# Optimization experiments

Hardware: AMD Instinct MI355X
Metric: run time of the kernel (lower is better)

Reference implementation:

```python
import jax, jax.numpy as jnp
import numpy as np

N_USERS = 100_000
N_ITEMS = 100_000
D = 64            # args.in_size == args.out_size (GraphConv has weight=None)
N_INTENTS = 128   # hardcoded in DCCF
HID = 128         # SemanticAttention hidden_size
N_UI_EDGES = 1_000_000
N_MP_EDGES = 500_000
N_MP = 2          # metapaths per node type
B = 4096
N_LAYERS = 2      # hardcoded in DCCF


def setup_inputs() -> dict:
    key = jax.random.key(0)
    ks = jax.random.split(key, 20)
    s = 0.1
    inp = {}
    inp['user_feat'] = jax.random.normal(ks[0], (N_USERS, D), jnp.float32) * s
    inp['item_feat'] = jax.random.normal(ks[1], (N_ITEMS, D), jnp.float32) * s
    inp['user_intent'] = jax.random.normal(ks[2], (D, N_INTENTS), jnp.float32) * s
    inp['item_intent'] = jax.random.normal(ks[3], (D, N_INTENTS), jnp.float32) * s
    inp['sa_u_W1'] = jax.random.normal(ks[4], (D, HID), jnp.float32) * s
    inp['sa_u_b1'] = jnp.zeros((HID,), jnp.float32)
    inp['sa_u_w2'] = jax.random.normal(ks[5], (HID,), jnp.float32) * s
    inp['sa_i_W1'] = jax.random.normal(ks[6], (D, HID), jnp.float32) * s
    inp['sa_i_b1'] = jnp.zeros((HID,), jnp.float32)
    inp['sa_i_w2'] = jax.random.normal(ks[7], (HID,), jnp.float32) * s
    inp['ui_src'] = jax.random.randint(ks[8], (N_UI_EDGES,), 0, N_USERS)
    inp['ui_dst'] = jax.random.randint(ks[9], (N_UI_EDGES,), 0, N_ITEMS)
    inp['mp_user'] = jax.random.randint(ks[10], (N_MP, 2, N_MP_EDGES), 0, N_USERS)
    inp['mp_item'] = jax.random.randint(ks[11], (N_MP, 2, N_MP_EDGES), 0, N_ITEMS)
    # indices drawn WITHOUT replacement so torch.unique(index) in ssl_loss is a no-op
    inp['user_idx'] = jax.random.choice(ks[12], N_USERS, (B,), replace=False)
    inp['item_idx'] = jax.random.choice(ks[13], N_ITEMS, (B,), replace=False)
    inp['neg_item_idx'] = jax.random.randint(ks[14], (B,), 0, N_ITEMS)
    return inp


def _forward(user_feat, item_feat, user_intent, item_intent,
             sa_u_W1, sa_u_b1, sa_u_w2, sa_i_W1, sa_i_b1, sa_i_w2,
             ui_src, ui_dst, mp_user, mp_item, user_idx, item_idx, neg_item_idx):
    n_nodes = N_USERS + N_ITEMS
    # symmetric bipartite adjacency in COO (tmp_adj + tmp_adj.T)
    rows = jnp.concatenate([ui_src, ui_dst + N_USERS])
    cols = jnp.concatenate([ui_dst + N_USERS, ui_src])
    deg = jnp.maximum(jax.ops.segment_sum(jnp.ones_like(rows, jnp.float32), rows,
                                          num_segments=n_nodes), 1.0)
    dinv = jax.lax.rsqrt(deg)
    gv = dinv[rows] * dinv[cols]  # G = D^{-1/2} A D^{-1/2}

    def spmm(x):  # gather-scale-scatter, the torch_sparse.spmm
        return jax.ops.segment_sum(gv[:, None] * x[cols], rows, num_segments=n_nodes)

    # ---- DCCF ----
    emb = jnp.concatenate([user_feat, item_feat], axis=0)
    total = emb
    for _ in range(N_LAYERS):
        gnn = spmm(emb)
        u, it = emb[:N_USERS], emb[N_USERS:]
        u_int = jax.nn.softmax(u @ user_intent, axis=1) @ user_intent.T
        i_int = jax.nn.softmax(it @ item_intent, axis=1) @ item_intent.T
        emb = gnn + jnp.concatenate([u_int, i_int], axis=0) + emb
        total = total + emb  # torch.stack(...).sum(dim=1)
    ua, ia = total[:N_USERS], total[N_USERS:]

    # ---- HANLayer: GraphConv(norm='both', weight=None) per metapath ----
    def graphconv(src, dst, h, n):
        ones = jnp.ones_like(src, jnp.float32)
        outdeg = jnp.maximum(jax.ops.segment_sum(ones, src, num_segments=n), 1.0)
        indeg = jnp.maximum(jax.ops.segment_sum(ones, dst, num_segments=n), 1.0)
        x = h * jax.lax.rsqrt(outdeg)[:, None]
        agg = jax.ops.segment_sum(x[src], dst, num_segments=n)
        return agg * jax.lax.rsqrt(indeg)[:, None]

    def sem_att(z, W1, b1, w2):  # z: [N, M, D]
        w = jnp.mean(jnp.tanh(z @ W1 + b1) @ w2, axis=0)  # [M]
        beta = jax.nn.softmax(w)
        return jnp.einsum('m,nmd->nd', beta, z)

    zu = jnp.stack([graphconv(mp_user[m, 0], mp_user[m, 1], user_feat, N_USERS)
                    for m in range(N_MP)], axis=1)
    h2_u = sem_att(zu, sa_u_W1, sa_u_b1, sa_u_w2)
    zi = jnp.stack([graphconv(mp_item[m, 0], mp_item[m, 1], item_feat, N_ITEMS)
                    for m in range(N_MP)], axis=1)
    h2_i = sem_att(zi, sa_i_W1, sa_i_b1, sa_i_w2)

    user_emb = 0.5 * ua + 0.5 * h2_u
    item_emb = 0.5 * ia + 0.5 * h2_i

    def ssl(d1, d2, idx):  # InfoNCE with temp 0.5 (idx already unique)
        e1 = d1[idx]
        e2 = d2[idx]
        e1 = e1 / jnp.linalg.norm(e1, axis=1, keepdims=True)
        e2 = e2 / jnp.linalg.norm(e2, axis=1, keepdims=True)
        pos = jnp.sum(e1 * e2, axis=1) / 0.5
        lse = jax.nn.logsumexp(e1 @ e2.T / 0.5, axis=1)
        return -jnp.sum(pos - lse) / idx.shape[0]

    ssl_loss = ssl(h2_u, ua, user_idx) + ssl(h2_i, ia, item_idx)
    return (user_emb[user_idx], item_emb[item_idx], item_emb[neg_item_idx], ssl_loss)


def reference(user_feat, item_feat, user_intent, item_intent,
              sa_u_W1, sa_u_b1, sa_u_w2, sa_i_W1, sa_i_b1, sa_i_w2,
              ui_src, ui_dst, mp_user, mp_item, user_idx, item_idx, neg_item_idx):
    return _forward(user_feat, item_feat, user_intent, item_intent,
                    sa_u_W1, sa_u_b1, sa_u_w2, sa_i_W1, sa_i_b1, sa_i_w2,
                    ui_src, ui_dst, mp_user, mp_item, user_idx, item_idx, neg_item_idx)
```

## Files before the change

### kernel.cpp

```cpp
#include <hip/hip_runtime.h>
#include <math.h>

#define NUSERS   100000
#define NITEMS   100000
#define NNODES   200000
#define DD       64
#define NI       128
#define E_UI     1000000
#define E_MP     500000
#define BB       4096
#define NSTRIP   6250

#define O_CNT       0LL
#define O_OUTCNT    600000LL
#define O_CURSOR    1000000LL
#define O_PARTIALS  1600000LL
#define O_UITB_U    1625600LL
#define O_UITB_I    1629696LL
#define O_UIB_U     1633792LL
#define O_UIB_I     1637888LL
#define O_W1B_U     1641984LL
#define O_W1B_I     1646080LL
#define O_SUMEXP    1700000LL
#define O_POS       1708192LL
#define ZEND        1716384LL
#define O_OFF       1716384LL
#define O_BSUM      2316448LL
#define O_DINV      2317472LL
#define O_OINV      2517472LL
#define O_IINV      2917472LL
#define O_ADJ       3317472LL
#define O_WSUM      7317472LL
#define O_EMBA      7317480LL
#define O_TOTAL     20117480LL
#define O_EMBB      32917480LL
#define O_E1U       45717480LL
#define O_E2U       45979624LL
#define O_E1I       46241768LL
#define O_E2I       46503912LL

typedef __attribute__((ext_vector_type(8))) short short8;
typedef __attribute__((ext_vector_type(4))) float f32x4;

__device__ __forceinline__ short f2bf(float x) {
  unsigned u = __float_as_uint(x);
  unsigned r = (u + 0x7FFFu + ((u >> 16) & 1u)) >> 16;
  return (short)r;
}

__global__ void k_hist_main(const int* __restrict__ src, const int* __restrict__ dst,
                            int* __restrict__ cnt) {
  int e = blockIdx.x * 256 + threadIdx.x;
  if (e < E_UI) {
    atomicAdd(&cnt[src[e]], 1);
    atomicAdd(&cnt[NUSERS + dst[e]], 1);
  }
}

__global__ void k_hist_mp(const int* __restrict__ mpu, const int* __restrict__ mpi,
                          int* __restrict__ cnt, int* __restrict__ outcnt) {
  int e = blockIdx.x * 256 + threadIdx.x;
  int g = blockIdx.y;
  if (e < E_MP) {
    const int* base = (g < 2) ? (mpu + (long long)g * 2 * E_MP)
                              : (mpi + (long long)(g - 2) * 2 * E_MP);
    int s = base[e];
    int d = base[E_MP + e];
    atomicAdd(&outcnt[g * NUSERS + s], 1);
    atomicAdd(&cnt[NNODES + g * NUSERS + d], 1);
  }
}

__global__ __launch_bounds__(1024) void k_scan1(const int* __restrict__ in, int* __restrict__ out,
                                                int* __restrict__ bsum, int n) {
  __shared__ int s[1024];
  int i = blockIdx.x * 1024 + threadIdx.x;
  int v = (i < n) ? in[i] : 0;
  s[threadIdx.x] = v;
  __syncthreads();
  for (int off = 1; off < 1024; off <<= 1) {
    int x = (threadIdx.x >= off) ? s[threadIdx.x - off] : 0;
    __syncthreads();
    s[threadIdx.x] += x;
    __syncthreads();
  }
  if (i < n) out[i] = s[threadIdx.x] - v;
  if (threadIdx.x == 1023) bsum[blockIdx.x] = s[1023];
}

__global__ __launch_bounds__(1024) void k_scan2(int* __restrict__ bsum, int nb) {
  __shared__ int s[1024];
  int v = (threadIdx.x < nb) ? bsum[threadIdx.x] : 0;
  s[threadIdx.x] = v;
  __syncthreads();
  for (int off = 1; off < 1024; off <<= 1) {
    int x = (threadIdx.x >= off) ? s[threadIdx.x - off] : 0;
    __syncthreads();
    s[threadIdx.x] += x;
    __syncthreads();
  }
  if (threadIdx.x < nb) bsum[threadIdx.x] = s[threadIdx.x] - v;
}

__global__ __launch_bounds__(1024) void k_scan3(int* __restrict__ out, const int* __restrict__ bsum, int n) {
  int i = blockIdx.x * 1024 + threadIdx.x;
  if (i < n) out[i] += bsum[blockIdx.x];
}

__global__ void k_inv(const int* __restrict__ cnt, const int* __restrict__ outcnt,
                      float* __restrict__ dinv, float* __restrict__ iinv, float* __restrict__ oinv) {
  int i = blockIdx.x * 256 + threadIdx.x;
  if (i < NNODES) {
    int c = cnt[i]; if (c < 1) c = 1;
    dinv[i] = 1.0f / sqrtf((float)c);
  } else if (i < 600000) {
    int c = cnt[i]; if (c < 1) c = 1;
    iinv[i - NNODES] = 1.0f / sqrtf((float)c);
  }
  if (i < 400000) {
    int c = outcnt[i]; if (c < 1) c = 1;
    oinv[i] = 1.0f / sqrtf((float)c);
  }
}

__global__ void k_scatter_main(const int* __restrict__ src, const int* __restrict__ dst,
                               const int* __restrict__ off, int* __restrict__ cursor,
                               int* __restrict__ adj) {
  int e = blockIdx.x * 256 + threadIdx.x;
  if (e < E_UI) {
    int u = src[e];
    int it = NUSERS + dst[e];
    int p = atomicAdd(&cursor[u], 1);
    adj[off[u] + p] = it;
    int q = atomicAdd(&cursor[it], 1);
    adj[off[it] + q] = u;
  }
}

__global__ void k_scatter_mp(const int* __restrict__ mpu, const int* __restrict__ mpi,
                             const int* __restrict__ off, int* __restrict__ cursor,
                             int* __restrict__ adj) {
  int e = blockIdx.x * 256 + threadIdx.x;
  int g = blockIdx.y;
  if (e < E_MP) {
    const int* base = (g < 2) ? (mpu + (long long)g * 2 * E_MP)
                              : (mpi + (long long)(g - 2) * 2 * E_MP);
    int s = base[e];
    int d = base[E_MP + e];
    int node = NNODES + g * NUSERS + d;
    int p = atomicAdd(&cursor[node], 1);
    adj[off[node] + p] = s;
  }
}

__global__ void k_init(const float4* __restrict__ uf, const float4* __restrict__ itf,
                       float4* __restrict__ emb) {
  int i = blockIdx.x * 256 + threadIdx.x;
  if (i < 3200000) {
    emb[i] = (i < 1600000) ? uf[i] : itf[i - 1600000];
  }
}

__global__ void k_tw(const float* __restrict__ UIu, const float* __restrict__ UIi,
                     const float* __restrict__ W1u, const float* __restrict__ W1i,
                     short* __restrict__ UITBu, short* __restrict__ UITBi,
                     short* __restrict__ UIBu,  short* __restrict__ UIBi,
                     short* __restrict__ W1Bu,  short* __restrict__ W1Bi) {
  int t = blockIdx.x * 256 + threadIdx.x;
  if (t < 8192) {
    int d = t >> 7, j = t & 127;
    UITBu[j * 64 + d] = f2bf(UIu[t]);
    UITBi[j * 64 + d] = f2bf(UIi[t]);
    UIBu[t] = f2bf(UIu[t]);
    UIBi[t] = f2bf(UIi[t]);
    W1Bu[j * 64 + d] = f2bf(W1u[t]);
    W1Bi[j * 64 + d] = f2bf(W1i[t]);
  }
}

__device__ __forceinline__ float acc8(const float* __restrict__ tbl, int miv, float mwv,
                                      int rem, int lane, float acc) {
  unsigned wb = __float_as_uint(mwv);
  for (int k = 0; k < rem; k += 8) {
    int n0 = __builtin_amdgcn_readlane(miv, k + 0);
    int n1 = __builtin_amdgcn_readlane(miv, k + 1);
    int n2 = __builtin_amdgcn_readlane(miv, k + 2);
    int n3 = __builtin_amdgcn_readlane(miv, k + 3);
    int n4 = __builtin_amdgcn_readlane(miv, k + 4);
    int n5 = __builtin_amdgcn_readlane(miv, k + 5);
    int n6 = __builtin_amdgcn_readlane(miv, k + 6);
    int n7 = __builtin_amdgcn_readlane(miv, k + 7);
    float w0 = __uint_as_float(__builtin_amdgcn_readlane(wb, k + 0));
    float w1 = __uint_as_float(__builtin_amdgcn_readlane(wb, k + 1));
    float w2 = __uint_as_float(__builtin_amdgcn_readlane(wb, k + 2));
    float w3 = __uint_as_float(__builtin_amdgcn_readlane(wb, k + 3));
    float w4 = __uint_as_float(__builtin_amdgcn_readlane(wb, k + 4));
    float w5 = __uint_as_float(__builtin_amdgcn_readlane(wb, k + 5));
    float w6 = __uint_as_float(__builtin_amdgcn_readlane(wb, k + 6));
    float w7 = __uint_as_float(__builtin_amdgcn_readlane(wb, k + 7));
    float v0 = tbl[((long long)n0 << 6) + lane], v1 = tbl[((long long)n1 << 6) + lane];
    float v2 = tbl[((long long)n2 << 6) + lane], v3 = tbl[((long long)n3 << 6) + lane];
    float v4 = tbl[((long long)n4 << 6) + lane], v5 = tbl[((long long)n5 << 6) + lane];
    float v6 = tbl[((long long)n6 << 6) + lane], v7 = tbl[((long long)n7 << 6) + lane];
    acc += w0 * v0; acc += w1 * v1; acc += w2 * v2; acc += w3 * v3;
    acc += w4 * v4; acc += w5 * v5; acc += w6 * v6; acc += w7 * v7;
  }
  return acc;
}

__device__ __forceinline__ float gather_tail(const float* __restrict__ tbl,
                                             const int* __restrict__ adj,
                                             int start, int c,
                                             const float* __restrict__ warr, int wofs,
                                             int lane, float acc) {
  for (int kb = 64; kb < c; kb += 64) {
    int rem = c - kb; if (rem > 64) rem = 64;
    int ti = 0; float tw = 0.0f;
    if (lane < rem) { ti = adj[start + kb + lane]; tw = warr[wofs + ti]; }
    acc = acc8(tbl, ti, tw, rem, lane, acc);
  }
  return acc;
}

__device__ __forceinline__ void acc4x(const float* __restrict__ tbl, int miv, float mwv,
                                      int rem, int grp, int dq, f32x4& acc) {
  for (int k = 0; k < rem; k += 16) {
    int s0 = k + grp, s1 = k + 4 + grp, s2 = k + 8 + grp, s3 = k + 12 + grp;
    int n0 = __shfl(miv, s0), n1 = __shfl(miv, s1);
    int n2 = __shfl(miv, s2), n3 = __shfl(miv, s3);
    float w0 = __shfl(mwv, s0), w1 = __shfl(mwv, s1);
    float w2 = __shfl(mwv, s2), w3 = __shfl(mwv, s3);
    float4 v0 = *(const float4*)(tbl + ((long long)n0 << 6) + dq);
    float4 v1 = *(const float4*)(tbl + ((long long)n1 << 6) + dq);
    float4 v2 = *(const float4*)(tbl + ((long long)n2 << 6) + dq);
    float4 v3 = *(const float4*)(tbl + ((long long)n3 << 6) + dq);
    acc.x += w0 * v0.x; acc.y += w0 * v0.y; acc.z += w0 * v0.z; acc.w += w0 * v0.w;
    acc.x += w1 * v1.x; acc.y += w1 * v1.y; acc.z += w1 * v1.z; acc.w += w1 * v1.w;
    acc.x += w2 * v2.x; acc.y += w2 * v2.y; acc.z += w2 * v2.z; acc.w += w2 * v2.w;
    acc.x += w3 * v3.x; acc.y += w3 * v3.y; acc.z += w3 * v3.z; acc.w += w3 * v3.w;
  }
}

__device__ __forceinline__ void gather_tail4(const float* __restrict__ tbl,
                                             const int* __restrict__ adj,
                                             int start, int c,
                                             const float* __restrict__ warr, int wofs,
                                             int lane, int grp, int dq, f32x4& acc) {
  for (int kb = 64; kb < c; kb += 64) {
    int rem = c - kb; if (rem > 64) rem = 64;
    int ti = 0; float tw = 0.0f;
    if (lane < rem) { ti = adj[start + kb + lane]; tw = warr[wofs + ti]; }
    acc4x(tbl, ti, tw, rem, grp, dq, acc);
  }
}

__device__ __forceinline__ float bcastf(float x) {
  return __uint_as_float(__builtin_amdgcn_readfirstlane(__float_as_uint(x)));
}

__global__ __launch_bounds__(256, 4) void k_layer(
    const float* __restrict__ ecur, float* __restrict__ enext, float* __restrict__ total,
    const int* __restrict__ adj, const int* __restrict__ off, const int* __restrict__ cnt,
    const float* __restrict__ dinv,
    const short* __restrict__ UITBu, const short* __restrict__ UITBi,
    const short* __restrict__ UIBu,  const short* __restrict__ UIBi, int layer) {
  __shared__ float sZ[4][16 * 68];
  __shared__ short sP[4][16 * 136];
  int w = threadIdx.x >> 6, lane = threadIdx.x & 63;
  int nb = blockIdx.x * 64 + w * 16;
  const short* UITB = (nb < NUSERS) ? UITBu : UITBi;
  const short* UIB  = (nb < NUSERS) ? UIBu  : UIBi;
  float* rowZ = sZ[w];
  short* rowP = sP[w];

#pragma unroll
  for (int h = 0; h < 2; h++) {
    int nb8 = nb + h * 8;
    int ofs[8], cns[8];
    float dn[8];
    int mi[8]; float mw[8];
#pragma unroll
    for (int m = 0; m < 8; m++) {
      ofs[m] = __builtin_amdgcn_readfirstlane(off[nb8 + m]);
      cns[m] = __builtin_amdgcn_readfirstlane(cnt[nb8 + m]);
      dn[m]  = bcastf(dinv[nb8 + m]);
    }
#pragma unroll
    for (int m = 0; m < 8; m++)
      mi[m] = (lane < cns[m]) ? adj[ofs[m] + lane] : 0;
#pragma unroll
    for (int m = 0; m < 8; m++)
      mw[m] = (lane < cns[m]) ? dinv[mi[m]] : 0.0f;
#pragma unroll
    for (int m = 0; m < 8; m++) {
      int c = cns[m];
      int rem = c < 64 ? c : 64;
      float acc = acc8(ecur, mi[m], mw[m], rem, lane, 0.0f);
      if (c > 64) acc = gather_tail(ecur, adj, ofs[m], c, dinv, 0, lane, acc);
      rowZ[(h * 8 + m) * 68 + lane] = dn[m] * acc;
    }
  }

  int quad = lane >> 4, mrow = lane & 15;
  const float* vrow = ecur + (((long long)(nb + mrow)) << 6) + quad * 8;
  float4 va0 = *(const float4*)(vrow);
  float4 va1 = *(const float4*)(vrow + 4);
  float4 vc0 = *(const float4*)(vrow + 32);
  float4 vc1 = *(const float4*)(vrow + 36);
  short8 a0 = { f2bf(va0.x), f2bf(va0.y), f2bf(va0.z), f2bf(va0.w),
                f2bf(va1.x), f2bf(va1.y), f2bf(va1.z), f2bf(va1.w) };
  short8 a1 = { f2bf(vc0.x), f2bf(vc0.y), f2bf(vc0.z), f2bf(vc0.w),
                f2bf(vc1.x), f2bf(vc1.y), f2bf(vc1.z), f2bf(vc1.w) };
  float den0 = 0.f, den1 = 0.f, den2 = 0.f, den3 = 0.f;
  short* pw = rowP + (quad * 4) * 136 + mrow;
#pragma unroll
  for (int jt = 0; jt < 8; jt++) {
    const short* wr = UITB + ((jt * 16 + mrow) << 6) + quad * 8;
    short8 b0 = *(const short8*)(wr);
    short8 bh = *(const short8*)(wr + 32);
    f32x4 acc = {0.f, 0.f, 0.f, 0.f};
    acc = __builtin_amdgcn_mfma_f32_16x16x32_bf16(a0, b0, acc, 0, 0, 0);
    acc = __builtin_amdgcn_mfma_f32_16x16x32_bf16(a1, bh, acc, 0, 0, 0);
    float e0 = __expf(acc[0]), e1 = __expf(acc[1]);
    float e2 = __expf(acc[2]), e3 = __expf(acc[3]);
    den0 += e0; den1 += e1; den2 += e2; den3 += e3;
    short* pj = pw + jt * 16;
    pj[0] = f2bf(e0); pj[136] = f2bf(e1); pj[272] = f2bf(e2); pj[408] = f2bf(e3);
  }
  for (int mask = 1; mask <= 8; mask <<= 1) {
    den0 += __shfl_xor(den0, mask); den1 += __shfl_xor(den1, mask);
    den2 += __shfl_xor(den2, mask); den3 += __shfl_xor(den3, mask);
  }
  float rd0 = 1.f / den0, rd1 = 1.f / den1, rd2 = 1.f / den2, rd3 = 1.f / den3;

#pragma unroll
  for (int dt = 0; dt < 4; dt++) {
    f32x4 acc = {0.f, 0.f, 0.f, 0.f};
#pragma unroll
    for (int c = 0; c < 4; c++) {
      const short* pr = rowP + mrow * 136 + c * 32 + quad * 8;
      short8 af = *(const short8*)(pr);
      const short* br = UIB + ((dt * 16 + mrow) << 7) + c * 32 + quad * 8;
      short8 bf = *(const short8*)(br);
      acc = __builtin_amdgcn_mfma_f32_16x16x32_bf16(af, bf, acc, 0, 0, 0);
    }
    int d = dt * 16 + mrow;
#define COMB(r, rd)                                                            \
    { int node = nb + quad * 4 + r;                                            \
      long long base = (((long long)node) << 6) + d;                           \
      float o = acc[r] * rd;                                                   \
      float gn = rowZ[(quad * 4 + r) * 68 + d];                                \
      float vv = ecur[base];                                                   \
      float ne = gn + o + vv;                                                  \
      enext[base] = ne;                                                        \
      total[base] = (layer == 0) ? (vv + ne) : (total[base] + ne); }
    COMB(0, rd0) COMB(1, rd1) COMB(2, rd2) COMB(3, rd3)
#undef COMB
  }
}

__global__ __launch_bounds__(256, 6) void k_mp_gather(
    const float* __restrict__ uf, const float* __restrict__ itf,
    const int* __restrict__ adj, const int* __restrict__ off, const int* __restrict__ cnt,
    const float* __restrict__ oinv, const float* __restrict__ iinv,
    float* __restrict__ zu, float* __restrict__ zi) {
  int g = blockIdx.y;
  const float* feat = (g < 2) ? uf : itf;
  float* zb = (g < 2) ? zu + ((long long)g * NUSERS << 6)
                      : zi + ((long long)(g - 2) * NUSERS << 6);
  int w = threadIdx.x >> 6, lane = threadIdx.x & 63;
  int n0 = (blockIdx.x * 4 + w) * 8;
  int gofs = g * NUSERS;
  int grp = lane >> 4, dq = (lane & 15) << 2;
  int ofs[8], cns[8];
  float iv[8];
  int mi[8]; float mw[8];
#pragma unroll
  for (int m = 0; m < 8; m++) {
    int node = NNODES + gofs + n0 + m;
    ofs[m] = __builtin_amdgcn_readfirstlane(off[node]);
    cns[m] = __builtin_amdgcn_readfirstlane(cnt[node]);
    iv[m]  = bcastf(iinv[gofs + n0 + m]);
  }
#pragma unroll
  for (int m = 0; m < 8; m++)
    mi[m] = (lane < cns[m]) ? adj[ofs[m] + lane] : 0;
#pragma unroll
  for (int m = 0; m < 8; m++)
    mw[m] = (lane < cns[m]) ? oinv[gofs + mi[m]] : 0.0f;
#pragma unroll
  for (int m = 0; m < 8; m++) {
    int c = cns[m];
    int rem = c < 64 ? c : 64;
    f32x4 acc = {0.f, 0.f, 0.f, 0.f};
    acc4x(feat, mi[m], mw[m], rem, grp, dq, acc);
    if (c > 64) gather_tail4(feat, adj, ofs[m], c, oinv, gofs, lane, grp, dq, acc);
    acc.x += __shfl_xor(acc.x, 16); acc.y += __shfl_xor(acc.y, 16);
    acc.z += __shfl_xor(acc.z, 16); acc.w += __shfl_xor(acc.w, 16);
    acc.x += __shfl_xor(acc.x, 32); acc.y += __shfl_xor(acc.y, 32);
    acc.z += __shfl_xor(acc.z, 32); acc.w += __shfl_xor(acc.w, 32);
    if (lane < 16) {
      float s = iv[m];
      float4 o = { acc.x * s, acc.y * s, acc.z * s, acc.w * s };
      *(float4*)&zb[((long long)(n0 + m) << 6) + dq] = o;
    }
  }
}

__global__ __launch_bounds__(256, 4) void k_mp_mlp(
    const float* __restrict__ zu, const float* __restrict__ zi,
    const short* __restrict__ W1Bu, const float* __restrict__ b1u, const float* __restrict__ w2u,
    const short* __restrict__ W1Bi, const float* __restrict__ b1i, const float* __restrict__ w2i,
    float* __restrict__ partials) {
  int g = blockIdx.y;
  const short* W1B = (g < 2) ? W1Bu : W1Bi;
  const float* b1  = (g < 2) ? b1u : b1i;
  const float* w2  = (g < 2) ? w2u : w2i;
  const float* zb  = (g < 2) ? zu + ((long long)g * NUSERS << 6)
                             : zi + ((long long)(g - 2) * NUSERS << 6);
  int w = threadIdx.x >> 6, lane = threadIdx.x & 63;
  int strip = blockIdx.x * 4 + w;
  if (strip >= NSTRIP) return;
  int quad = lane >> 4, mrow = lane & 15;
  const float* zrow = zb + (((long long)(strip * 16 + mrow)) << 6) + quad * 8;
  float4 za0 = *(const float4*)(zrow);
  float4 za1 = *(const float4*)(zrow + 4);
  float4 zc0 = *(const float4*)(zrow + 32);
  float4 zc1 = *(const float4*)(zrow + 36);
  short8 a0 = { f2bf(za0.x), f2bf(za0.y), f2bf(za0.z), f2bf(za0.w),
                f2bf(za1.x), f2bf(za1.y), f2bf(za1.z), f2bf(za1.w) };
  short8 a1 = { f2bf(zc0.x), f2bf(zc0.y), f2bf(zc0.z), f2bf(zc0.w),
                f2bf(zc1.x), f2bf(zc1.y), f2bf(zc1.z), f2bf(zc1.w) };
  float psum = 0.0f;
#pragma unroll
  for (int jt = 0; jt < 8; jt++) {
    const short* wr = W1B + ((jt * 16 + mrow) << 6) + quad * 8;
    short8 b0 = *(const short8*)(wr);
    short8 bh = *(const short8*)(wr + 32);
    f32x4 acc = {0.f, 0.f, 0.f, 0.f};
    acc = __builtin_amdgcn_mfma_f32_16x16x32_bf16(a0, b0, acc, 0, 0, 0);
    acc = __builtin_amdgcn_mfma_f32_16x16x32_bf16(a1, bh, acc, 0, 0, 0);
    int j = jt * 16 + mrow;
    float bj = b1[j], wj = w2[j];
#pragma unroll
    for (int r = 0; r < 4; r++) {
      float s = acc[r] + bj;
      psum += wj * (1.0f - 2.0f / (__expf(2.0f * s) + 1.0f));
    }
  }
  for (int m = 32; m; m >>= 1) psum += __shfl_xor(psum, m);
  if (lane == 0) partials[g * NSTRIP + strip] = psum;
}

__global__ void k_beta(const float* __restrict__ partials, float* __restrict__ wsum) {
  int g = blockIdx.x;
  float s = 0.0f;
  for (int i = threadIdx.x; i < NSTRIP; i += 256) s += partials[g * NSTRIP + i];
  for (int m = 32; m; m >>= 1) s += __shfl_xor(s, m);
  __shared__ float r[4];
  if ((threadIdx.x & 63) == 0) r[threadIdx.x >> 6] = s;
  __syncthreads();
  if (threadIdx.x == 0) wsum[g] = r[0] + r[1] + r[2] + r[3];
}

__global__ __launch_bounds__(256) void k_h2out(
    const float* __restrict__ zu, const float* __restrict__ zi,
    const int* __restrict__ user_idx, const int* __restrict__ item_idx, const int* __restrict__ neg_idx,
    const float* __restrict__ total,
    const float* __restrict__ wsum, float* __restrict__ out,
    float* __restrict__ e1u, float* __restrict__ e2u,
    float* __restrict__ e1i, float* __restrict__ e2i, float* __restrict__ pos) {
  int lane = threadIdx.x & 63;
  int row = (blockIdx.x << 2) + (threadIdx.x >> 6);
  int seg = row >> 12;
  int r = row & 4095;
  int idx;
  const float* zb;
  int gbase;
  if (seg == 0)      { idx = user_idx[r]; zb = zu; gbase = 0; }
  else if (seg == 1) { idx = item_idx[r]; zb = zi; gbase = 2; }
  else               { idx = neg_idx[r];  zb = zi; gbase = 2; }
  int tnode = gbase ? (NUSERS + idx) : idx;
  float t = total[((long long)tnode << 6) + lane];
  float w0 = wsum[gbase] * (1.0f / 100000.0f);
  float w1 = wsum[gbase + 1] * (1.0f / 100000.0f);
  float mb = fmaxf(w0, w1);
  float b0 = expf(w0 - mb), b1 = expf(w1 - mb);
  float bs = b0 + b1;
  b0 /= bs; b1 /= bs;
  float z0 = zb[((long long)idx << 6) + lane];
  float z1 = zb[(((long long)NUSERS + idx) << 6) + lane];
  float h2 = b0 * z0 + b1 * z1;
  out[((long long)row << 6) + lane] = 0.5f * t + 0.5f * h2;
  if (seg < 2) {
    float n1 = h2 * h2, n2 = t * t;
    for (int m = 32; m; m >>= 1) { n1 += __shfl_xor(n1, m); n2 += __shfl_xor(n2, m); }
    n1 = sqrtf(n1); n2 = sqrtf(n2);
    float a = h2 / n1, b = t / n2;
    float d = a * b;
    for (int m = 32; m; m >>= 1) d += __shfl_xor(d, m);
    float* e1 = seg ? e1i : e1u;
    float* e2 = seg ? e2i : e2u;
    e1[((long long)r << 6) + lane] = a;
    e2[((long long)r << 6) + lane] = b;
    if (lane == 0) pos[seg * BB + r] = 2.0f * d;
  }
}

__global__ __launch_bounds__(256) void k_gemm(const float* __restrict__ e1u, const float* __restrict__ e2u,
                                              const float* __restrict__ e1i, const float* __restrict__ e2i,
                                              float* __restrict__ sumexp) {
  int side = blockIdx.z;
  const float* A = side ? e1i : e1u;
  const float* Bm = side ? e2i : e2u;
  __shared__ float sA[64][68], sB[64][68];
  int bb = blockIdx.y, kk = blockIdx.x;
  int tid = threadIdx.x;
  for (int i = tid; i < 1024; i += 256) {
    int row = i >> 4, d4 = (i & 15) << 2;
    float4 a = *(const float4*)&A[(((long long)(bb * 64 + row)) << 6) + d4];
    float4 b = *(const float4*)&Bm[(((long long)(kk * 64 + row)) << 6) + d4];
    *(float4*)&sA[row][d4] = a;
    *(float4*)&sB[row][d4] = b;
  }
  __syncthreads();
  int tx = tid & 15, ty = tid >> 4;
  int r0 = ty << 2, c0 = tx << 2;
  float acc[4][4] = {{0}};
  for (int k = 0; k < 64; k += 4) {
    float4 a0 = *(const float4*)&sA[r0 + 0][k];
    float4 a1 = *(const float4*)&sA[r0 + 1][k];
    float4 a2 = *(const float4*)&sA[r0 + 2][k];
    float4 a3 = *(const float4*)&sA[r0 + 3][k];
    float4 b0 = *(const float4*)&sB[c0 + 0][k];
    float4 b1 = *(const float4*)&sB[c0 + 1][k];
    float4 b2 = *(const float4*)&sB[c0 + 2][k];
    float4 b3 = *(const float4*)&sB[c0 + 3][k];
#define DOT(u_, v_) (u_.x*v_.x + u_.y*v_.y + u_.z*v_.z + u_.w*v_.w)
    acc[0][0] += DOT(a0, b0); acc[0][1] += DOT(a0, b1); acc[0][2] += DOT(a0, b2); acc[0][3] += DOT(a0, b3);
    acc[1][0] += DOT(a1, b0); acc[1][1] += DOT(a1, b1); acc[1][2] += DOT(a1, b2); acc[1][3] += DOT(a1, b3);
    acc[2][0] += DOT(a2, b0); acc[2][1] += DOT(a2, b1); acc[2][2] += DOT(a2, b2); acc[2][3] += DOT(a2, b3);
    acc[3][0] += DOT(a3, b0); acc[3][1] += DOT(a3, b1); acc[3][2] += DOT(a3, b2); acc[3][3] += DOT(a3, b3);
#undef DOT
  }
#pragma unroll
  for (int i = 0; i < 4; i++) {
    float rs = __expf(2.0f * acc[i][0]) + __expf(2.0f * acc[i][1])
             + __expf(2.0f * acc[i][2]) + __expf(2.0f * acc[i][3]);
    for (int m = 1; m < 16; m <<= 1) rs += __shfl_xor(rs, m);
    if (tx == 0)
      __hip_atomic_fetch_add(&sumexp[side * BB + bb * 64 + r0 + i], rs,
                             __ATOMIC_RELAXED, __HIP_MEMORY_SCOPE_AGENT);
  }
}

__global__ void k_loss(const float* __restrict__ sumexp, const float* __restrict__ pos,
                       float* __restrict__ out) {
  float s = 0.0f;
  for (int i = threadIdx.x; i < 2 * BB; i += 256) s += logf(sumexp[i]) - pos[i];
  for (int m = 32; m; m >>= 1) s += __shfl_xor(s, m);
  __shared__ float r[4];
  if ((threadIdx.x & 63) == 0) r[threadIdx.x >> 6] = s;
  __syncthreads();
  if (threadIdx.x == 0) out[3 * BB * DD] = (r[0] + r[1] + r[2] + r[3]) * (1.0f / (float)BB);
}

extern "C" void kernel_launch(void* const* d_in, const int* in_sizes, int n_in,
                              void* d_out, int out_size, void* d_ws, size_t ws_size,
                              hipStream_t stream) {
  const float* uf  = (const float*)d_in[0];
  const float* itf = (const float*)d_in[1];
  const float* UIu = (const float*)d_in[2];
  const float* UIi = (const float*)d_in[3];
  const float* W1u = (const float*)d_in[4];
  const float* b1u = (const float*)d_in[5];
  const float* w2u = (const float*)d_in[6];
  const float* W1i = (const float*)d_in[7];
  const float* b1i = (const float*)d_in[8];
  const float* w2i = (const float*)d_in[9];
  const int* ui_src   = (const int*)d_in[10];
  const int* ui_dst   = (const int*)d_in[11];
  const int* mpu      = (const int*)d_in[12];
  const int* mpi      = (const int*)d_in[13];
  const int* user_idx = (const int*)d_in[14];
  const int* item_idx = (const int*)d_in[15];
  const int* neg_idx  = (const int*)d_in[16];
  float* out = (float*)d_out;

  float* wf = (float*)d_ws;
  int*   wi = (int*)d_ws;

  int*   cnt      = wi + O_CNT;
  int*   outcnt   = wi + O_OUTCNT;
  int*   cursor   = wi + O_CURSOR;
  float* partials = wf + O_PARTIALS;
  short* UITBu    = (short*)(wf + O_UITB_U);
  short* UITBi    = (short*)(wf + O_UITB_I);
  short* UIBu     = (short*)(wf + O_UIB_U);
  short* UIBi     = (short*)(wf + O_UIB_I);
  short* W1Bu     = (short*)(wf + O_W1B_U);
  short* W1Bi     = (short*)(wf + O_W1B_I);
  float* sumexp   = wf + O_SUMEXP;
  float* pos      = wf + O_POS;
  int*   off      = wi + O_OFF;
  int*   bsum     = wi + O_BSUM;
  float* dinv     = wf + O_DINV;
  float* oinv     = wf + O_OINV;
  float* iinv     = wf + O_IINV;
  int*   adj      = wi + O_ADJ;
  float* wsum     = wf + O_WSUM;
  float* emba     = wf + O_EMBA;
  float* total    = wf + O_TOTAL;
  float* embb     = wf + O_EMBB;
  float* e1u      = wf + O_E1U;
  float* e2u      = wf + O_E2U;
  float* e1i      = wf + O_E1I;
  float* e2i      = wf + O_E2I;

  hipMemsetAsync(d_ws, 0, (size_t)ZEND * 4, stream);

  k_hist_main<<<(E_UI + 255) / 256, 256, 0, stream>>>(ui_src, ui_dst, cnt);
  k_hist_mp<<<dim3((E_MP + 255) / 256, 4), 256, 0, stream>>>(mpu, mpi, cnt, outcnt);

  const int NSCAN = 600000;
  const int NB = (NSCAN + 1023) / 1024;
  k_scan1<<<NB, 1024, 0, stream>>>(cnt, off, bsum, NSCAN);
  k_scan2<<<1, 1024, 0, stream>>>(bsum, NB);
  k_scan3<<<NB, 1024, 0, stream>>>(off, bsum, NSCAN);

  k_inv<<<(600000 + 255) / 256, 256, 0, stream>>>(cnt, outcnt, dinv, iinv, oinv);

  k_scatter_main<<<(E_UI + 255) / 256, 256, 0, stream>>>(ui_src, ui_dst, off, cursor, adj);
  k_scatter_mp<<<dim3((E_MP + 255) / 256, 4), 256, 0, stream>>>(mpu, mpi, off, cursor, adj);

  k_init<<<(3200000 + 255) / 256, 256, 0, stream>>>((const float4*)uf, (const float4*)itf,
                                                    (float4*)emba);
  k_tw<<<32, 256, 0, stream>>>(UIu, UIi, W1u, W1i, UITBu, UITBi, UIBu, UIBi, W1Bu, W1Bi);

  k_layer<<<3125, 256, 0, stream>>>(emba, embb, total, adj, off, cnt, dinv,
                                    UITBu, UITBi, UIBu, UIBi, 0);
  k_layer<<<3125, 256, 0, stream>>>(embb, emba, total, adj, off, cnt, dinv,
                                    UITBu, UITBi, UIBu, UIBi, 1);

  k_mp_gather<<<dim3(3125, 4), 256, 0, stream>>>(uf, itf, adj, off, cnt, oinv, iinv,
                                                 emba, embb);
  k_mp_mlp<<<dim3((NSTRIP + 3) / 4, 4), 256, 0, stream>>>(emba, embb, W1Bu, b1u, w2u,
                                                          W1Bi, b1i, w2i, partials);
  k_beta<<<4, 256, 0, stream>>>(partials, wsum);

  k_h2out<<<3072, 256, 0, stream>>>(emba, embb, user_idx, item_idx, neg_idx, total,
                                    wsum, out, e1u, e2u, e1i, e2i, pos);

  k_gemm<<<dim3(64, 64, 2), 256, 0, stream>>>(e1u, e2u, e1i, e2i, sumexp);
  k_loss<<<1, 256, 0, stream>>>(sumexp, pos, out);
}
```

Measured before the change: 1.232 ms.

## Use bf16 MFMA for SSL logsumexp GEMM, regroup layer gathers, shrink mp_gather blocks

The SSL similarity GEMM now stores normalized embeddings as bf16 and computes the 4096x4096 logits with MFMA 16x16x32 instructions straight from registers, replacing the fp32 shared-memory FMA tile. This cuts GEMM ALU and shared-memory cost, at some cost in precision of the logits. The layer kernel now issues the A-fragment loads before a single 16-node gather loop instead of two 8-node halves, which adds latency overlap but raises register pressure. k_mp_gather handles 4 nodes per wave instead of 8 with twice the blocks, which should improve load balance and occupancy.

```diff
diff --git a/kernel.cpp b/kernel.cpp
--- a/kernel.cpp
+++ b/kernel.cpp
@@ -272,36 +272,8 @@
   const short* UIB  = (nb < NUSERS) ? UIBu  : UIBi;
   float* rowZ = sZ[w];
   short* rowP = sP[w];
-
-#pragma unroll
-  for (int h = 0; h < 2; h++) {
-    int nb8 = nb + h * 8;
-    int ofs[8], cns[8];
-    float dn[8];
-    int mi[8]; float mw[8];
-#pragma unroll
-    for (int m = 0; m < 8; m++) {
-      ofs[m] = __builtin_amdgcn_readfirstlane(off[nb8 + m]);
-      cns[m] = __builtin_amdgcn_readfirstlane(cnt[nb8 + m]);
-      dn[m]  = bcastf(dinv[nb8 + m]);
-    }
-#pragma unroll
-    for (int m = 0; m < 8; m++)
-      mi[m] = (lane < cns[m]) ? adj[ofs[m] + lane] : 0;
-#pragma unroll
-    for (int m = 0; m < 8; m++)
-      mw[m] = (lane < cns[m]) ? dinv[mi[m]] : 0.0f;
-#pragma unroll
-    for (int m = 0; m < 8; m++) {
-      int c = cns[m];
-      int rem = c < 64 ? c : 64;
-      float acc = acc8(ecur, mi[m], mw[m], rem, lane, 0.0f);
-      if (c > 64) acc = gather_tail(ecur, adj, ofs[m], c, dinv, 0, lane, acc);
-      rowZ[(h * 8 + m) * 68 + lane] = dn[m] * acc;
-    }
-  }
-
   int quad = lane >> 4, mrow = lane & 15;
+
   const float* vrow = ecur + (((long long)(nb + mrow)) << 6) + quad * 8;
   float4 va0 = *(const float4*)(vrow);
   float4 va1 = *(const float4*)(vrow + 4);
@@ -311,6 +283,33 @@
                 f2bf(va1.x), f2bf(va1.y), f2bf(va1.z), f2bf(va1.w) };
   short8 a1 = { f2bf(vc0.x), f2bf(vc0.y), f2bf(vc0.z), f2bf(vc0.w),
                 f2bf(vc1.x), f2bf(vc1.y), f2bf(vc1.z), f2bf(vc1.w) };
+
+  {
+    int ofs[16], cns[16];
+    float dn[16];
+    int mi[16]; float mw[16];
+#pragma unroll
+    for (int m = 0; m < 16; m++) {
+      ofs[m] = __builtin_amdgcn_readfirstlane(off[nb + m]);
+      cns[m] = __builtin_amdgcn_readfirstlane(cnt[nb + m]);
+      dn[m]  = bcastf(dinv[nb + m]);
+    }
+#pragma unroll
+    for (int m = 0; m < 16; m++)
+      mi[m] = (lane < cns[m]) ? adj[ofs[m] + lane] : 0;
+#pragma unroll
+    for (int m = 0; m < 16; m++)
+      mw[m] = (lane < cns[m]) ? dinv[mi[m]] : 0.0f;
+#pragma unroll
+    for (int m = 0; m < 16; m++) {
+      int c = cns[m];
+      int rem = c < 64 ? c : 64;
+      float acc = acc8(ecur, mi[m], mw[m], rem, lane, 0.0f);
+      if (c > 64) acc = gather_tail(ecur, adj, ofs[m], c, dinv, 0, lane, acc);
+      rowZ[m * 68 + lane] = dn[m] * acc;
+    }
+  }
+
   float den0 = 0.f, den1 = 0.f, den2 = 0.f, den3 = 0.f;
   short* pw = rowP + (quad * 4) * 136 + mrow;
 #pragma unroll
@@ -369,27 +368,27 @@
   float* zb = (g < 2) ? zu + ((long long)g * NUSERS << 6)
                       : zi + ((long long)(g - 2) * NUSERS << 6);
   int w = threadIdx.x >> 6, lane = threadIdx.x & 63;
-  int n0 = (blockIdx.x * 4 + w) * 8;
+  int n0 = (blockIdx.x * 4 + w) * 4;
   int gofs = g * NUSERS;
   int grp = lane >> 4, dq = (lane & 15) << 2;
-  int ofs[8], cns[8];
-  float iv[8];
-  int mi[8]; float mw[8];
-#pragma unroll
-  for (int m = 0; m < 8; m++) {
+  int ofs[4], cns[4];
+  float iv[4];
+  int mi[4]; float mw[4];
+#pragma unroll
+  for (int m = 0; m < 4; m++) {
     int node = NNODES + gofs + n0 + m;
     ofs[m] = __builtin_amdgcn_readfirstlane(off[node]);
     cns[m] = __builtin_amdgcn_readfirstlane(cnt[node]);
     iv[m]  = bcastf(iinv[gofs + n0 + m]);
   }
 #pragma unroll
-  for (int m = 0; m < 8; m++)
+  for (int m = 0; m < 4; m++)
     mi[m] = (lane < cns[m]) ? adj[ofs[m] + lane] : 0;
 #pragma unroll
-  for (int m = 0; m < 8; m++)
+  for (int m = 0; m < 4; m++)
     mw[m] = (lane < cns[m]) ? oinv[gofs + mi[m]] : 0.0f;
 #pragma unroll
-  for (int m = 0; m < 8; m++) {
+  for (int m = 0; m < 4; m++) {
     int c = cns[m];
     int rem = c < 64 ? c : 64;
     f32x4 acc = {0.f, 0.f, 0.f, 0.f};
@@ -468,8 +467,8 @@
     const int* __restrict__ user_idx, const int* __restrict__ item_idx, const int* __restrict__ neg_idx,
     const float* __restrict__ total,
     const float* __restrict__ wsum, float* __restrict__ out,
-    float* __restrict__ e1u, float* __restrict__ e2u,
-    float* __restrict__ e1i, float* __restrict__ e2i, float* __restrict__ pos) {
+    short* __restrict__ e1u, short* __restrict__ e2u,
+    short* __restrict__ e1i, short* __restrict__ e2i, float* __restrict__ pos) {
   int lane = threadIdx.x & 63;
   int row = (blockIdx.x << 2) + (threadIdx.x >> 6);
   int seg = row >> 12;
@@ -499,58 +498,78 @@
     float a = h2 / n1, b = t / n2;
     float d = a * b;
     for (int m = 32; m; m >>= 1) d += __shfl_xor(d, m);
-    float* e1 = seg ? e1i : e1u;
-    float* e2 = seg ? e2i : e2u;
-    e1[((long long)r << 6) + lane] = a;
-    e2[((long long)r << 6) + lane] = b;
+    short* e1 = seg ? e1i : e1u;
+    short* e2 = seg ? e2i : e2u;
+    e1[((long long)r << 6) + lane] = f2bf(a);
+    e2[((long long)r << 6) + lane] = f2bf(b);
     if (lane == 0) pos[seg * BB + r] = 2.0f * d;
   }
 }
 
-__global__ __launch_bounds__(256) void k_gemm(const float* __restrict__ e1u, const float* __restrict__ e2u,
-                                              const float* __restrict__ e1i, const float* __restrict__ e2i,
+__global__ __launch_bounds__(256) void k_gemm(const short* __restrict__ e1u, const short* __restrict__ e2u,
+                                              const short* __restrict__ e1i, const short* __restrict__ e2i,
                                               float* __restrict__ sumexp) {
   int side = blockIdx.z;
-  const float* A = side ? e1i : e1u;
-  const float* Bm = side ? e2i : e2u;
-  __shared__ float sA[64][68], sB[64][68];
-  int bb = blockIdx.y, kk = blockIdx.x;
-  int tid = threadIdx.x;
-  for (int i = tid; i < 1024; i += 256) {
-    int row = i >> 4, d4 = (i & 15) << 2;
-    float4 a = *(const float4*)&A[(((long long)(bb * 64 + row)) << 6) + d4];
-    float4 b = *(const float4*)&Bm[(((long long)(kk * 64 + row)) << 6) + d4];
-    *(float4*)&sA[row][d4] = a;
-    *(float4*)&sB[row][d4] = b;
-  }
-  __syncthreads();
-  int tx = tid & 15, ty = tid >> 4;
-  int r0 = ty << 2, c0 = tx << 2;
-  float acc[4][4] = {{0}};
-  for (int k = 0; k < 64; k += 4) {
-    float4 a0 = *(const float4*)&sA[r0 + 0][k];
-    float4 a1 = *(const float4*)&sA[r0 + 1][k];
-    float4 a2 = *(const float4*)&sA[r0 + 2][k];
-    float4 a3 = *(const float4*)&sA[r0 + 3][k];
-    float4 b0 = *(const float4*)&sB[c0 + 0][k];
-    float4 b1 = *(const float4*)&sB[c0 + 1][k];
-    float4 b2 = *(const float4*)&sB[c0 + 2][k];
-    float4 b3 = *(const float4*)&sB[c0 + 3][k];
-#define DOT(u_, v_) (u_.x*v_.x + u_.y*v_.y + u_.z*v_.z + u_.w*v_.w)
-    acc[0][0] += DOT(a0, b0); acc[0][1] += DOT(a0, b1); acc[0][2] += DOT(a0, b2); acc[0][3] += DOT(a0, b3);
-    acc[1][0] += DOT(a1, b0); acc[1][1] += DOT(a1, b1); acc[1][2] += DOT(a1, b2); acc[1][3] += DOT(a1, b3);
-    acc[2][0] += DOT(a2, b0); acc[2][1] += DOT(a2, b1); acc[2][2] += DOT(a2, b2); acc[2][3] += DOT(a2, b3);
-    acc[3][0] += DOT(a3, b0); acc[3][1] += DOT(a3, b1); acc[3][2] += DOT(a3, b2); acc[3][3] += DOT(a3, b3);
-#undef DOT
-  }
-#pragma unroll
-  for (int i = 0; i < 4; i++) {
-    float rs = __expf(2.0f * acc[i][0]) + __expf(2.0f * acc[i][1])
-             + __expf(2.0f * acc[i][2]) + __expf(2.0f * acc[i][3]);
-    for (int m = 1; m < 16; m <<= 1) rs += __shfl_xor(rs, m);
-    if (tx == 0)
-      __hip_atomic_fetch_add(&sumexp[side * BB + bb * 64 + r0 + i], rs,
-                             __ATOMIC_RELAXED, __HIP_MEMORY_SCOPE_AGENT);
+  const short* A = side ? e1i : e1u;
+  const short* B = side ? e2i : e2u;
+  int w = threadIdx.x >> 6, lane = threadIdx.x & 63;
+  int quad = lane >> 4, mrow = lane & 15;
+  int rbase = blockIdx.y * 64;
+  int cbase = blockIdx.x * 256 + w * 64;
+
+  short8 a0[4], a1[4], b0[4], b1[4];
+#pragma unroll
+  for (int ri = 0; ri < 4; ri++) {
+    const short* ar = A + ((long long)(rbase + ri * 16 + mrow) << 6) + quad * 8;
+    a0[ri] = *(const short8*)ar;
+    a1[ri] = *(const short8*)(ar + 32);
+  }
+#pragma unroll
+  for (int ci = 0; ci < 4; ci++) {
+    const short* br = B + ((long long)(cbase + ci * 16 + mrow) << 6) + quad * 8;
+    b0[ci] = *(const short8*)br;
+    b1[ci] = *(const short8*)(br + 32);
+  }
+  float rs0[4] = {0.f, 0.f, 0.f, 0.f};
+  float rs1[4] = {0.f, 0.f, 0.f, 0.f};
+  float rs2[4] = {0.f, 0.f, 0.f, 0.f};
+  float rs3[4] = {0.f, 0.f, 0.f, 0.f};
+#pragma unroll
+  for (int ri = 0; ri < 4; ri++) {
+#pragma unroll
+    for (int ci = 0; ci < 4; ci++) {
+      f32x4 acc = {0.f, 0.f, 0.f, 0.f};
+      acc = __builtin_amdgcn_mfma_f32_16x16x32_bf16(a0[ri], b0[ci], acc, 0, 0, 0);
+      acc = __builtin_amdgcn_mfma_f32_16x16x32_bf16(a1[ri], b1[ci], acc, 0, 0, 0);
+      float e0 = __expf(2.0f * acc[0]);
+      float e1 = __expf(2.0f * acc[1]);
+      float e2 = __expf(2.0f * acc[2]);
+      float e3 = __expf(2.0f * acc[3]);
+      if (ri == 0) { rs0[0] += e0; rs0[1] += e1; rs0[2] += e2; rs0[3] += e3; }
+      if (ri == 1) { rs1[0] += e0; rs1[1] += e1; rs1[2] += e2; rs1[3] += e3; }
+      if (ri == 2) { rs2[0] += e0; rs2[1] += e1; rs2[2] += e2; rs2[3] += e3; }
+      if (ri == 3) { rs3[0] += e0; rs3[1] += e1; rs3[2] += e2; rs3[3] += e3; }
+    }
+  }
+#pragma unroll
+  for (int mask = 1; mask <= 8; mask <<= 1) {
+#pragma unroll
+    for (int r = 0; r < 4; r++) {
+      rs0[r] += __shfl_xor(rs0[r], mask);
+      rs1[r] += __shfl_xor(rs1[r], mask);
+      rs2[r] += __shfl_xor(rs2[r], mask);
+      rs3[r] += __shfl_xor(rs3[r], mask);
+    }
+  }
+  if (mrow == 0) {
+    float* sb = sumexp + side * BB + rbase + quad * 4;
+#pragma unroll
+    for (int r = 0; r < 4; r++) {
+      __hip_atomic_fetch_add(&sb[r], rs0[r], __ATOMIC_RELAXED, __HIP_MEMORY_SCOPE_AGENT);
+      __hip_atomic_fetch_add(&sb[16 + r], rs1[r], __ATOMIC_RELAXED, __HIP_MEMORY_SCOPE_AGENT);
+      __hip_atomic_fetch_add(&sb[32 + r], rs2[r], __ATOMIC_RELAXED, __HIP_MEMORY_SCOPE_AGENT);
+      __hip_atomic_fetch_add(&sb[48 + r], rs3[r], __ATOMIC_RELAXED, __HIP_MEMORY_SCOPE_AGENT);
+    }
   }
 }
 
@@ -612,10 +631,10 @@
   float* emba     = wf + O_EMBA;
   float* total    = wf + O_TOTAL;
   float* embb     = wf + O_EMBB;
-  float* e1u      = wf + O_E1U;
-  float* e2u      = wf + O_E2U;
-  float* e1i      = wf + O_E1I;
-  float* e2i      = wf + O_E2I;
+  short* e1u      = (short*)(wf + O_E1U);
+  short* e2u      = (short*)(wf + O_E2U);
+  short* e1i      = (short*)(wf + O_E1I);
+  short* e2i      = (short*)(wf + O_E2I);
 
   hipMemsetAsync(d_ws, 0, (size_t)ZEND * 4, stream);
 
@@ -642,7 +661,7 @@
   k_layer<<<3125, 256, 0, stream>>>(embb, emba, total, adj, off, cnt, dinv,
                                     UITBu, UITBi, UIBu, UIBi, 1);
 
-  k_mp_gather<<<dim3(3125, 4), 256, 0, stream>>>(uf, itf, adj, off, cnt, oinv, iinv,
+  k_mp_gather<<<dim3(6250, 4), 256, 0, stream>>>(uf, itf, adj, off, cnt, oinv, iinv,
                                                  emba, embb);
   k_mp_mlp<<<dim3((NSTRIP + 3) / 4, 4), 256, 0, stream>>>(emba, embb, W1Bu, b1u, w2u,
                                                           W1Bi, b1i, w2i, partials);
@@ -651,6 +670,6 @@
   k_h2out<<<3072, 256, 0, stream>>>(emba, embb, user_idx, item_idx, neg_idx, total,
                                     wsum, out, e1u, e2u, e1i, e2i, pos);
 
-  k_gemm<<<dim3(64, 64, 2), 256, 0, stream>>>(e1u, e2u, e1i, e2i, sumexp);
+  k_gemm<<<dim3(16, 64, 2), 256, 0, stream>>>(e1u, e2u, e1i, e2i, sumexp);
   k_loss<<<1, 256, 0, stream>>>(sumexp, pos, out);
 }
```

Result: faster. 1.175 ms (-4.6%).
